# Kernel tuning notes

Hardware: AMD Instinct MI355X
Metric: run time of the kernel (lower is better)

The kernel has to match this reference:

```python
import jax, jax.numpy as jnp
import numpy as np

B, H, KV, HD, D, S = 8, 32, 8, 128, 4096, 4096
PAST = S - 2  # 4094, cache nearly full
ROPE_THETA = 10000.0


def rotate_half(x):
    h = x.shape[-1] // 2
    return jnp.concatenate([-x[..., h:], x[..., :h]], axis=-1)


def setup_inputs() -> dict:
    key = jax.random.key(0)
    ks = jax.random.split(key, 10)
    hidden_states = jax.random.normal(ks[0], (B, 1, D), jnp.float32)
    # HF additive causal mask for decode: 0 where position is valid, -inf-ish beyond
    pos = jnp.arange(S)
    attention_mask = jnp.broadcast_to(
        jnp.where(pos < PAST + 1, 0.0, -1e9).astype(jnp.float32)[None, None, None, :],
        (B, 1, 1, S),
    )
    # RoPE cos/sin for the single decoded position (position id = PAST)
    inv_freq = 1.0 / (ROPE_THETA ** (jnp.arange(0, HD, 2, dtype=jnp.float32) / HD))
    ang = PAST * inv_freq  # [HD/2]
    emb = jnp.concatenate([ang, ang], axis=-1)  # [HD]
    cos = jnp.broadcast_to(jnp.cos(emb)[None, None, :], (B, 1, HD)).astype(jnp.float32)
    sin = jnp.broadcast_to(jnp.sin(emb)[None, None, :], (B, 1, HD)).astype(jnp.float32)
    past_key = jax.random.normal(ks[1], (B, KV, PAST, HD), jnp.float32)
    past_value = jax.random.normal(ks[2], (B, KV, PAST, HD), jnp.float32)
    k_cache = jax.random.normal(ks[3], (B, KV, S, HD), jnp.float32)
    v_cache = jax.random.normal(ks[4], (B, KV, S, HD), jnp.float32)
    Wq = jax.random.normal(ks[5], (D, H * HD), jnp.float32) * 0.02
    Wk = jax.random.normal(ks[6], (D, KV * HD), jnp.float32) * 0.02
    Wv = jax.random.normal(ks[7], (D, KV * HD), jnp.float32) * 0.02
    Wo = jax.random.normal(ks[8], (H * HD, D), jnp.float32) * 0.02
    return dict(hidden_states=hidden_states, attention_mask=attention_mask, cos=cos,
                sin=sin, past_key=past_key, past_value=past_value,
                k_cache=k_cache, v_cache=v_cache, Wq=Wq, Wk=Wk, Wv=Wv, Wo=Wo)


def reference(hidden_states, attention_mask, cos, sin, past_key, past_value,
              k_cache, v_cache, Wq, Wk, Wv, Wo):
    b = hidden_states.shape[0]
    past_len = past_key.shape[2]  # static
    # q/k/v projections for the single decode token
    q = (hidden_states @ Wq).reshape(b, 1, H, HD).transpose(0, 2, 1, 3)   # [B,H,1,hd]
    k = (hidden_states @ Wk).reshape(b, 1, KV, HD).transpose(0, 2, 1, 3)  # [B,KV,1,hd]
    v = (hidden_states @ Wv).reshape(b, 1, KV, HD).transpose(0, 2, 1, 3)
    # rotary: cos/sin [B,1,hd] -> unsqueeze head dim -> [B,1,1,hd]
    c = cos[:, None, :, :]
    s = sin[:, None, :, :]
    q = q * c + rotate_half(q) * s
    k = k * c + rotate_half(k) * s
    # StaticCache: scatter past K/V into positions [0, past_len), new token at past_len
    kf = k_cache.at[:, :, :past_len, :].set(past_key)
    kf = kf.at[:, :, past_len:past_len + 1, :].set(k)
    vf = v_cache.at[:, :, :past_len, :].set(past_value)
    vf = vf.at[:, :, past_len:past_len + 1, :].set(v)
    # GQA: repeat kv heads
    n_rep = H // KV
    kr = jnp.repeat(kf, n_rep, axis=1)  # [B,H,S,hd]
    vr = jnp.repeat(vf, n_rep, axis=1)
    scores = jnp.einsum('bhqd,bhkd->bhqk', q, kr) / np.float32(np.sqrt(HD))
    scores = scores + attention_mask  # [B,1,1,S] broadcasts over heads
    probs = jax.nn.softmax(scores.astype(jnp.float32), axis=-1).astype(q.dtype)
    out = jnp.einsum('bhqk,bhkd->bhqd', probs, vr)  # [B,H,1,hd]
    out = out.transpose(0, 2, 1, 3).reshape(b, 1, H * HD)
    return out @ Wo  # [B,1,D]
```

## Files before the change

kernel.cpp:

```cpp
#include <hip/hip_runtime.h>

#define BB 8
#define HH 32
#define KVH 8
#define HD 128
#define DD 4096
#define PAST 4094
#define QCOLS 4096
#define KVCOLS 1024
#define NC_QKV 6144
#define DCH 64
#define NDCH 64
#define CHUNK 64
#define NCHUNK 64
#define QSCALE 0.08838834764831845f

__global__ __launch_bounds__(256)
void matvec_partial(const float* __restrict__ hin,
                    const float* __restrict__ W0,
                    const float* __restrict__ W1,
                    const float* __restrict__ W2,
                    int c_w1, int c_w2, int NC,
                    float* __restrict__ part)
{
    __shared__ float hl[DCH][BB];
    const int tid = threadIdx.x;
    const int d0 = blockIdx.y * DCH;
    const int cb = blockIdx.x * 512;

    for (int idx = tid; idx < DCH * BB; idx += 256) {
        int dd = idx & (DCH - 1);
        int b = idx >> 6;
        hl[dd][b] = hin[b * DD + d0 + dd];
    }
    __syncthreads();

    const int c = cb + tid * 2;
    const float* W;
    int ldw, cl;
    if (c < c_w1)      { W = W0; ldw = c_w1;        cl = c; }
    else if (c < c_w2) { W = W1; ldw = c_w2 - c_w1; cl = c - c_w1; }
    else               { W = W2; ldw = NC - c_w2;   cl = c - c_w2; }
    const float* wp = W + (size_t)d0 * ldw + cl;

    float2 acc[BB];
    #pragma unroll
    for (int b = 0; b < BB; ++b) { acc[b].x = 0.f; acc[b].y = 0.f; }

    #pragma unroll 8
    for (int dd = 0; dd < DCH; ++dd) {
        float2 w = *(const float2*)wp;
        wp += ldw;
        float hv[8];
        *(float4*)&hv[0] = *(const float4*)&hl[dd][0];
        *(float4*)&hv[4] = *(const float4*)&hl[dd][4];
        #pragma unroll
        for (int b = 0; b < BB; ++b) {
            acc[b].x = fmaf(hv[b], w.x, acc[b].x);
            acc[b].y = fmaf(hv[b], w.y, acc[b].y);
        }
    }

    float* po = part + (size_t)blockIdx.y * (BB * NC) + c;
    #pragma unroll
    for (int b = 0; b < BB; ++b) {
        *(float2*)(po + (size_t)b * NC) = acc[b];
    }
}

#define FIN_PER_B 3584
__global__ __launch_bounds__(256)
void qkv_finish(const float* __restrict__ part,
                const float* __restrict__ cosv,
                const float* __restrict__ sinv,
                float* __restrict__ qout,
                float* __restrict__ knew,
                float* __restrict__ vnew)
{
    const int idx = blockIdx.x * 256 + threadIdx.x;
    const int b = idx / FIN_PER_B;
    const int r = idx - b * FIN_PER_B;

    if (r < 2560) {
        const int hd = r & 63;
        const int head = r >> 6;
        const int c_lo = head * HD + hd;
        const float* p0 = part + (size_t)b * NC_QKV + c_lo;
        const float* p1 = p0 + 64;
        float s_lo = 0.f, s_hi = 0.f;
        #pragma unroll 8
        for (int i = 0; i < NDCH; ++i) {
            s_lo += p0[(size_t)i * (BB * NC_QKV)];
            s_hi += p1[(size_t)i * (BB * NC_QKV)];
        }
        const float cs_lo = cosv[b * HD + hd];
        const float sn_lo = sinv[b * HD + hd];
        const float cs_hi = cosv[b * HD + hd + 64];
        const float sn_hi = sinv[b * HD + hd + 64];
        const float v_lo = fmaf(s_lo, cs_lo, -s_hi * sn_lo);
        const float v_hi = fmaf(s_hi, cs_hi,  s_lo * sn_hi);
        if (c_lo < QCOLS) {
            qout[b * QCOLS + c_lo]      = v_lo * QSCALE;
            qout[b * QCOLS + c_lo + 64] = v_hi * QSCALE;
        } else {
            knew[b * KVCOLS + (c_lo - QCOLS)]      = v_lo;
            knew[b * KVCOLS + (c_lo - QCOLS) + 64] = v_hi;
        }
    } else {
        const int c = r - 2560 + QCOLS + KVCOLS;
        const float* p = part + (size_t)b * NC_QKV + c;
        float s = 0.f;
        #pragma unroll 8
        for (int i = 0; i < NDCH; ++i) s += p[(size_t)i * (BB * NC_QKV)];
        vnew[b * KVCOLS + (c - QCOLS - KVCOLS)] = s;
    }
}

__global__ __launch_bounds__(256)
void attn_partial(const float* __restrict__ past_key,
                  const float* __restrict__ past_value,
                  const float* __restrict__ q,
                  const float* __restrict__ knew,
                  const float* __restrict__ vnew,
                  float* __restrict__ pacc,
                  float* __restrict__ pl)
{
    const int pair = blockIdx.x;
    const int wid = threadIdx.x >> 6;
    const int chunk = blockIdx.y * 4 + wid;
    const int b = pair >> 3;
    const int kv = pair & 7;
    const int lane = threadIdx.x & 63;
    const int half = lane >> 5;
    const int lh = lane & 31;

    const float* qb = q + b * QCOLS + (kv * 4) * HD + 4 * lh;
    const float4 qv0 = *(const float4*)(qb);
    const float4 qv1 = *(const float4*)(qb + HD);
    const float4 qv2 = *(const float4*)(qb + 2 * HD);
    const float4 qv3 = *(const float4*)(qb + 3 * HD);

    const float* kb = past_key   + (size_t)pair * PAST * HD;
    const float* vb = past_value + (size_t)pair * PAST * HD;

    float4 acc0 = {0,0,0,0}, acc1 = {0,0,0,0}, acc2 = {0,0,0,0}, acc3 = {0,0,0,0};
    float l0 = 0.f, l1 = 0.f, l2 = 0.f, l3 = 0.f;

    const int jbase = chunk * CHUNK + half;

    if (chunk < NCHUNK - 1) {
        const float* kp = kb + (size_t)jbase * HD + 4 * lh;
        const float* vp = vb + (size_t)jbase * HD + 4 * lh;
        #pragma unroll 4
        for (int it = 0; it < 32; ++it) {
            const float4 kk = *(const float4*)kp;  kp += 2 * HD;
            float s0 = kk.x*qv0.x + kk.y*qv0.y + kk.z*qv0.z + kk.w*qv0.w;
            float s1 = kk.x*qv1.x + kk.y*qv1.y + kk.z*qv1.z + kk.w*qv1.w;
            float s2 = kk.x*qv2.x + kk.y*qv2.y + kk.z*qv2.z + kk.w*qv2.w;
            float s3 = kk.x*qv3.x + kk.y*qv3.y + kk.z*qv3.z + kk.w*qv3.w;
            #pragma unroll
            for (int m = 1; m <= 16; m <<= 1) {
                s0 += __shfl_xor(s0, m, 64);
                s1 += __shfl_xor(s1, m, 64);
                s2 += __shfl_xor(s2, m, 64);
                s3 += __shfl_xor(s3, m, 64);
            }
            const float4 vv = *(const float4*)vp;  vp += 2 * HD;
            const float p0 = __expf(s0);
            const float p1 = __expf(s1);
            const float p2 = __expf(s2);
            const float p3 = __expf(s3);
            l0 += p0; l1 += p1; l2 += p2; l3 += p3;
            acc0.x = fmaf(p0, vv.x, acc0.x); acc0.y = fmaf(p0, vv.y, acc0.y);
            acc0.z = fmaf(p0, vv.z, acc0.z); acc0.w = fmaf(p0, vv.w, acc0.w);
            acc1.x = fmaf(p1, vv.x, acc1.x); acc1.y = fmaf(p1, vv.y, acc1.y);
            acc1.z = fmaf(p1, vv.z, acc1.z); acc1.w = fmaf(p1, vv.w, acc1.w);
            acc2.x = fmaf(p2, vv.x, acc2.x); acc2.y = fmaf(p2, vv.y, acc2.y);
            acc2.z = fmaf(p2, vv.z, acc2.z); acc2.w = fmaf(p2, vv.w, acc2.w);
            acc3.x = fmaf(p3, vv.x, acc3.x); acc3.y = fmaf(p3, vv.y, acc3.y);
            acc3.z = fmaf(p3, vv.z, acc3.z); acc3.w = fmaf(p3, vv.w, acc3.w);
        }
    } else {
        const float* kn = knew + pair * HD;
        const float* vn = vnew + pair * HD;
        #pragma unroll 2
        for (int it = 0; it < 32; ++it) {
            const int j = jbase + it * 2;
            const bool valid = (j <= PAST);
            const float* kp;
            const float* vp;
            if (j < PAST) { kp = kb + (size_t)j * HD; vp = vb + (size_t)j * HD; }
            else          { kp = kn;                   vp = vn; }

            const float4 kk = *(const float4*)(kp + 4 * lh);
            float s0 = kk.x*qv0.x + kk.y*qv0.y + kk.z*qv0.z + kk.w*qv0.w;
            float s1 = kk.x*qv1.x + kk.y*qv1.y + kk.z*qv1.z + kk.w*qv1.w;
            float s2 = kk.x*qv2.x + kk.y*qv2.y + kk.z*qv2.z + kk.w*qv2.w;
            float s3 = kk.x*qv3.x + kk.y*qv3.y + kk.z*qv3.z + kk.w*qv3.w;
            #pragma unroll
            for (int m = 1; m <= 16; m <<= 1) {
                s0 += __shfl_xor(s0, m, 64);
                s1 += __shfl_xor(s1, m, 64);
                s2 += __shfl_xor(s2, m, 64);
                s3 += __shfl_xor(s3, m, 64);
            }
            const float4 vv = *(const float4*)(vp + 4 * lh);
            const float p0 = valid ? __expf(s0) : 0.f;
            const float p1 = valid ? __expf(s1) : 0.f;
            const float p2 = valid ? __expf(s2) : 0.f;
            const float p3 = valid ? __expf(s3) : 0.f;
            l0 += p0; l1 += p1; l2 += p2; l3 += p3;
            acc0.x = fmaf(p0, vv.x, acc0.x); acc0.y = fmaf(p0, vv.y, acc0.y);
            acc0.z = fmaf(p0, vv.z, acc0.z); acc0.w = fmaf(p0, vv.w, acc0.w);
            acc1.x = fmaf(p1, vv.x, acc1.x); acc1.y = fmaf(p1, vv.y, acc1.y);
            acc1.z = fmaf(p1, vv.z, acc1.z); acc1.w = fmaf(p1, vv.w, acc1.w);
            acc2.x = fmaf(p2, vv.x, acc2.x); acc2.y = fmaf(p2, vv.y, acc2.y);
            acc2.z = fmaf(p2, vv.z, acc2.z); acc2.w = fmaf(p2, vv.w, acc2.w);
            acc3.x = fmaf(p3, vv.x, acc3.x); acc3.y = fmaf(p3, vv.y, acc3.y);
            acc3.z = fmaf(p3, vv.z, acc3.z); acc3.w = fmaf(p3, vv.w, acc3.w);
        }
    }

    l0 += __shfl_xor(l0, 32, 64);
    l1 += __shfl_xor(l1, 32, 64);
    l2 += __shfl_xor(l2, 32, 64);
    l3 += __shfl_xor(l3, 32, 64);
    acc0.x += __shfl_xor(acc0.x, 32, 64); acc0.y += __shfl_xor(acc0.y, 32, 64);
    acc0.z += __shfl_xor(acc0.z, 32, 64); acc0.w += __shfl_xor(acc0.w, 32, 64);
    acc1.x += __shfl_xor(acc1.x, 32, 64); acc1.y += __shfl_xor(acc1.y, 32, 64);
    acc1.z += __shfl_xor(acc1.z, 32, 64); acc1.w += __shfl_xor(acc1.w, 32, 64);
    acc2.x += __shfl_xor(acc2.x, 32, 64); acc2.y += __shfl_xor(acc2.y, 32, 64);
    acc2.z += __shfl_xor(acc2.z, 32, 64); acc2.w += __shfl_xor(acc2.w, 32, 64);
    acc3.x += __shfl_xor(acc3.x, 32, 64); acc3.y += __shfl_xor(acc3.y, 32, 64);
    acc3.z += __shfl_xor(acc3.z, 32, 64); acc3.w += __shfl_xor(acc3.w, 32, 64);

    if (half == 0) {
        float* po = pacc + (((size_t)pair * NCHUNK + chunk) * 4) * HD + 4 * lh;
        *(float4*)(po)          = acc0;
        *(float4*)(po + HD)     = acc1;
        *(float4*)(po + 2*HD)   = acc2;
        *(float4*)(po + 3*HD)   = acc3;
        if (lh == 0) {
            float* plo = pl + ((size_t)pair * NCHUNK + chunk) * 4;
            plo[0] = l0; plo[1] = l1; plo[2] = l2; plo[3] = l3;
        }
    }
}

__global__ __launch_bounds__(256)
void attn_combine(const float* __restrict__ pacc,
                  const float* __restrict__ pl,
                  float* __restrict__ attn_out)
{
    const int idx = blockIdx.x * 256 + threadIdx.x;
    const int d = idx & 127;
    const int h = (idx >> 7) & 31;
    const int b = idx >> 12;
    const int kv = h >> 2;
    const int qi = h & 3;
    const int pair = b * 8 + kv;

    const float* pa  = pacc + (((size_t)pair * NCHUNK) * 4 + qi) * HD + d;
    const float* pls = pl + (size_t)pair * NCHUNK * 4 + qi;
    float acc = 0.f, lsum = 0.f;
    #pragma unroll 8
    for (int c = 0; c < NCHUNK; ++c) {
        acc  += pa[(size_t)c * 4 * HD];
        lsum += pls[c * 4];
    }
    attn_out[b * QCOLS + h * HD + d] = acc / lsum;
}

__global__ __launch_bounds__(256)
void wo_finish(const float* __restrict__ part, float* __restrict__ out)
{
    const int idx = blockIdx.x * 256 + threadIdx.x;
    float s = 0.f;
    #pragma unroll 8
    for (int i = 0; i < NDCH; ++i) s += part[(size_t)i * (BB * QCOLS) + idx];
    out[idx] = s;
}

extern "C" void kernel_launch(void* const* d_in, const int* in_sizes, int n_in,
                              void* d_out, int out_size, void* d_ws, size_t ws_size,
                              hipStream_t stream)
{
    (void)in_sizes; (void)n_in; (void)out_size; (void)ws_size;
    const float* hidden     = (const float*)d_in[0];
    const float* cosv       = (const float*)d_in[2];
    const float* sinv       = (const float*)d_in[3];
    const float* past_key   = (const float*)d_in[4];
    const float* past_value = (const float*)d_in[5];
    const float* Wq = (const float*)d_in[8];
    const float* Wk = (const float*)d_in[9];
    const float* Wv = (const float*)d_in[10];
    const float* Wo = (const float*)d_in[11];
    float* out = (float*)d_out;
    float* ws  = (float*)d_ws;

    float* qkv_part = ws;
    float* qrope    = qkv_part + (size_t)NDCH * BB * NC_QKV;
    float* knew     = qrope + BB * QCOLS;
    float* vnew     = knew + BB * KVCOLS;
    float* pacc     = vnew + BB * KVCOLS;
    float* pl       = pacc + (size_t)64 * NCHUNK * 4 * HD;
    float* attn_out = pl + (size_t)64 * NCHUNK * 4;
    float* wo_part  = qkv_part;

    matvec_partial<<<dim3(12, NDCH), 256, 0, stream>>>(
        hidden, Wq, Wk, Wv, 4096, 5120, NC_QKV, qkv_part);
    qkv_finish<<<(BB * FIN_PER_B) / 256, 256, 0, stream>>>(
        qkv_part, cosv, sinv, qrope, knew, vnew);
    attn_partial<<<dim3(64, NCHUNK / 4), 256, 0, stream>>>(
        past_key, past_value, qrope, knew, vnew, pacc, pl);
    attn_combine<<<(BB * HH * HD) / 256, 256, 0, stream>>>(pacc, pl, attn_out);
    matvec_partial<<<dim3(8, NDCH), 256, 0, stream>>>(
        attn_out, Wo, Wo, Wo, 4096, 5120, QCOLS, wo_part);
    wo_finish<<<(BB * QCOLS) / 256, 256, 0, stream>>>(wo_part, out);
}
```

Before: 111.7 us.

## Fuse attention combine into partial kernel via last-block counter, enlarge chunks

Removes the separate attn_combine launch: each attention block increments a per-pair atomic counter, and the last of the 8 blocks for that pair reduces the partial accumulators and writes the normalized output. The counter is reset inside qkv_finish. Chunk sizes for both the matvec reduction dimension and the attention sequence are doubled, which halves partial buffers and finish-kernel reads but also halves grid parallelism. wo_finish is vectorized to float4. The changes trade one kernel launch and partial-buffer traffic for fewer blocks in flight plus the fence and atomic overhead.

```diff
diff --git a/kernel.cpp b/kernel.cpp
--- a/kernel.cpp
+++ b/kernel.cpp
@@ -9,10 +9,10 @@
 #define QCOLS 4096
 #define KVCOLS 1024
 #define NC_QKV 6144
-#define DCH 64
-#define NDCH 64
-#define CHUNK 64
-#define NCHUNK 64
+#define DCH 128
+#define NDCH 32
+#define CHUNK 128
+#define NCHUNK 32
 #define QSCALE 0.08838834764831845f
 
 __global__ __launch_bounds__(256)
@@ -30,7 +30,7 @@
 
     for (int idx = tid; idx < DCH * BB; idx += 256) {
         int dd = idx & (DCH - 1);
-        int b = idx >> 6;
+        int b = idx >> 7;
         hl[dd][b] = hin[b * DD + d0 + dd];
     }
     __syncthreads();
@@ -47,7 +47,7 @@
     #pragma unroll
     for (int b = 0; b < BB; ++b) { acc[b].x = 0.f; acc[b].y = 0.f; }
 
-    #pragma unroll 8
+    #pragma unroll 16
     for (int dd = 0; dd < DCH; ++dd) {
         float2 w = *(const float2*)wp;
         wp += ldw;
@@ -75,8 +75,11 @@
                 const float* __restrict__ sinv,
                 float* __restrict__ qout,
                 float* __restrict__ knew,
-                float* __restrict__ vnew)
-{
+                float* __restrict__ vnew,
+                int* __restrict__ cnt)
+{
+    if (blockIdx.x == 0 && threadIdx.x < 64) cnt[threadIdx.x] = 0;
+
     const int idx = blockIdx.x * 256 + threadIdx.x;
     const int b = idx / FIN_PER_B;
     const int r = idx - b * FIN_PER_B;
@@ -123,7 +126,9 @@
                   const float* __restrict__ knew,
                   const float* __restrict__ vnew,
                   float* __restrict__ pacc,
-                  float* __restrict__ pl)
+                  float* __restrict__ pl,
+                  int* __restrict__ cnt,
+                  float* __restrict__ attn_out)
 {
     const int pair = blockIdx.x;
     const int wid = threadIdx.x >> 6;
@@ -152,7 +157,7 @@
         const float* kp = kb + (size_t)jbase * HD + 4 * lh;
         const float* vp = vb + (size_t)jbase * HD + 4 * lh;
         #pragma unroll 4
-        for (int it = 0; it < 32; ++it) {
+        for (int it = 0; it < 64; ++it) {
             const float4 kk = *(const float4*)kp;  kp += 2 * HD;
             float s0 = kk.x*qv0.x + kk.y*qv0.y + kk.z*qv0.z + kk.w*qv0.w;
             float s1 = kk.x*qv1.x + kk.y*qv1.y + kk.z*qv1.z + kk.w*qv1.w;
@@ -184,7 +189,7 @@
         const float* kn = knew + pair * HD;
         const float* vn = vnew + pair * HD;
         #pragma unroll 2
-        for (int it = 0; it < 32; ++it) {
+        for (int it = 0; it < 64; ++it) {
             const int j = jbase + it * 2;
             const bool valid = (j <= PAST);
             const float* kp;
@@ -245,40 +250,44 @@
             plo[0] = l0; plo[1] = l1; plo[2] = l2; plo[3] = l3;
         }
     }
-}
-
-__global__ __launch_bounds__(256)
-void attn_combine(const float* __restrict__ pacc,
-                  const float* __restrict__ pl,
-                  float* __restrict__ attn_out)
-{
-    const int idx = blockIdx.x * 256 + threadIdx.x;
-    const int d = idx & 127;
-    const int h = (idx >> 7) & 31;
-    const int b = idx >> 12;
-    const int kv = h >> 2;
-    const int qi = h & 3;
-    const int pair = b * 8 + kv;
-
-    const float* pa  = pacc + (((size_t)pair * NCHUNK) * 4 + qi) * HD + d;
-    const float* pls = pl + (size_t)pair * NCHUNK * 4 + qi;
-    float acc = 0.f, lsum = 0.f;
-    #pragma unroll 8
-    for (int c = 0; c < NCHUNK; ++c) {
-        acc  += pa[(size_t)c * 4 * HD];
-        lsum += pls[c * 4];
-    }
-    attn_out[b * QCOLS + h * HD + d] = acc / lsum;
+
+    __threadfence();
+    __syncthreads();
+    __shared__ int lastf;
+    if (threadIdx.x == 0) lastf = (atomicAdd(&cnt[pair], 1) == 7);
+    __syncthreads();
+    if (lastf) {
+        __threadfence();
+        const int qi = threadIdx.x >> 6;
+        const int dp = (threadIdx.x & 63) * 2;
+        const float* pa  = pacc + ((size_t)pair * NCHUNK * 4 + qi) * HD + dp;
+        const float* pls = pl + (size_t)pair * NCHUNK * 4 + qi;
+        float ax = 0.f, ay = 0.f, lsum = 0.f;
+        #pragma unroll 8
+        for (int ch = 0; ch < NCHUNK; ++ch) {
+            const float2 t = *(const float2*)(pa + (size_t)ch * 4 * HD);
+            ax += t.x; ay += t.y;
+            lsum += pls[ch * 4];
+        }
+        const float inv = 1.f / lsum;
+        float* ao = attn_out + b * QCOLS + (kv * 4 + qi) * HD + dp;
+        float2 r; r.x = ax * inv; r.y = ay * inv;
+        *(float2*)ao = r;
+    }
 }
 
 __global__ __launch_bounds__(256)
 void wo_finish(const float* __restrict__ part, float* __restrict__ out)
 {
     const int idx = blockIdx.x * 256 + threadIdx.x;
-    float s = 0.f;
+    const float* p = part + (size_t)idx * 4;
+    float4 s = {0.f, 0.f, 0.f, 0.f};
     #pragma unroll 8
-    for (int i = 0; i < NDCH; ++i) s += part[(size_t)i * (BB * QCOLS) + idx];
-    out[idx] = s;
+    for (int i = 0; i < NDCH; ++i) {
+        const float4 t = *(const float4*)(p + (size_t)i * (BB * QCOLS));
+        s.x += t.x; s.y += t.y; s.z += t.z; s.w += t.w;
+    }
+    *(float4*)(out + (size_t)idx * 4) = s;
 }
 
 extern "C" void kernel_launch(void* const* d_in, const int* in_sizes, int n_in,
@@ -305,16 +314,16 @@
     float* pacc     = vnew + BB * KVCOLS;
     float* pl       = pacc + (size_t)64 * NCHUNK * 4 * HD;
     float* attn_out = pl + (size_t)64 * NCHUNK * 4;
+    int*   cnt      = (int*)(attn_out + BB * QCOLS);
     float* wo_part  = qkv_part;
 
     matvec_partial<<<dim3(12, NDCH), 256, 0, stream>>>(
         hidden, Wq, Wk, Wv, 4096, 5120, NC_QKV, qkv_part);
     qkv_finish<<<(BB * FIN_PER_B) / 256, 256, 0, stream>>>(
-        qkv_part, cosv, sinv, qrope, knew, vnew);
+        qkv_part, cosv, sinv, qrope, knew, vnew, cnt);
     attn_partial<<<dim3(64, NCHUNK / 4), 256, 0, stream>>>(
-        past_key, past_value, qrope, knew, vnew, pacc, pl);
-    attn_combine<<<(BB * HH * HD) / 256, 256, 0, stream>>>(pacc, pl, attn_out);
+        past_key, past_value, qrope, knew, vnew, pacc, pl, cnt, attn_out);
     matvec_partial<<<dim3(8, NDCH), 256, 0, stream>>>(
         attn_out, Wo, Wo, Wo, 4096, 5120, QCOLS, wo_part);
-    wo_finish<<<(BB * QCOLS) / 256, 256, 0, stream>>>(wo_part, out);
-}
+    wo_finish<<<(BB * QCOLS / 4) / 256, 256, 0, stream>>>(wo_part, out);
+}
```

Result: slower. 215.4 us (+92.9%).

## Restructure decode attention to one query head per 16-lane group, larger chunks

Applied to the files above, without the earlier changes.

The attention partial kernel now gives each 16-lane group one query head, and each lane holds 8 elements of head_dim. Previously each wave split keys across two halves, with every lane carrying all four GQA heads. Each lane now processes one key row per iteration, which shortens the shuffle reduction to 4 steps and removes the cross-half reduction and the per-row bounds check. Chunks grow to 128 keys, halving the number of partial results that attn_combine must merge; the new token is handled as a separate tail step. wo_finish is vectorised to float4 with a quarter of the threads, and unroll factors are raised in qkv_finish.

```diff
diff --git a/kernel.cpp b/kernel.cpp
--- a/kernel.cpp
+++ b/kernel.cpp
@@ -11,8 +11,8 @@
 #define NC_QKV 6144
 #define DCH 64
 #define NDCH 64
-#define CHUNK 64
-#define NCHUNK 64
+#define CHUNK 128
+#define NCHUNK 32
 #define QSCALE 0.08838834764831845f
 
 __global__ __launch_bounds__(256)
@@ -88,7 +88,7 @@
         const float* p0 = part + (size_t)b * NC_QKV + c_lo;
         const float* p1 = p0 + 64;
         float s_lo = 0.f, s_hi = 0.f;
-        #pragma unroll 8
+        #pragma unroll 16
         for (int i = 0; i < NDCH; ++i) {
             s_lo += p0[(size_t)i * (BB * NC_QKV)];
             s_hi += p1[(size_t)i * (BB * NC_QKV)];
@@ -110,7 +110,7 @@
         const int c = r - 2560 + QCOLS + KVCOLS;
         const float* p = part + (size_t)b * NC_QKV + c;
         float s = 0.f;
-        #pragma unroll 8
+        #pragma unroll 16
         for (int i = 0; i < NDCH; ++i) s += p[(size_t)i * (BB * NC_QKV)];
         vnew[b * KVCOLS + (c - QCOLS - KVCOLS)] = s;
     }
@@ -131,119 +131,72 @@
     const int b = pair >> 3;
     const int kv = pair & 7;
     const int lane = threadIdx.x & 63;
-    const int half = lane >> 5;
-    const int lh = lane & 31;
-
-    const float* qb = q + b * QCOLS + (kv * 4) * HD + 4 * lh;
-    const float4 qv0 = *(const float4*)(qb);
-    const float4 qv1 = *(const float4*)(qb + HD);
-    const float4 qv2 = *(const float4*)(qb + 2 * HD);
-    const float4 qv3 = *(const float4*)(qb + 3 * HD);
+    const int g = lane >> 4;
+    const int i = lane & 15;
+
+    const float* qb = q + b * QCOLS + (kv * 4 + g) * HD + 8 * i;
+    const float4 qa = *(const float4*)(qb);
+    const float4 qc = *(const float4*)(qb + 4);
 
     const float* kb = past_key   + (size_t)pair * PAST * HD;
     const float* vb = past_value + (size_t)pair * PAST * HD;
 
-    float4 acc0 = {0,0,0,0}, acc1 = {0,0,0,0}, acc2 = {0,0,0,0}, acc3 = {0,0,0,0};
-    float l0 = 0.f, l1 = 0.f, l2 = 0.f, l3 = 0.f;
-
-    const int jbase = chunk * CHUNK + half;
-
-    if (chunk < NCHUNK - 1) {
-        const float* kp = kb + (size_t)jbase * HD + 4 * lh;
-        const float* vp = vb + (size_t)jbase * HD + 4 * lh;
-        #pragma unroll 4
-        for (int it = 0; it < 32; ++it) {
-            const float4 kk = *(const float4*)kp;  kp += 2 * HD;
-            float s0 = kk.x*qv0.x + kk.y*qv0.y + kk.z*qv0.z + kk.w*qv0.w;
-            float s1 = kk.x*qv1.x + kk.y*qv1.y + kk.z*qv1.z + kk.w*qv1.w;
-            float s2 = kk.x*qv2.x + kk.y*qv2.y + kk.z*qv2.z + kk.w*qv2.w;
-            float s3 = kk.x*qv3.x + kk.y*qv3.y + kk.z*qv3.z + kk.w*qv3.w;
-            #pragma unroll
-            for (int m = 1; m <= 16; m <<= 1) {
-                s0 += __shfl_xor(s0, m, 64);
-                s1 += __shfl_xor(s1, m, 64);
-                s2 += __shfl_xor(s2, m, 64);
-                s3 += __shfl_xor(s3, m, 64);
-            }
-            const float4 vv = *(const float4*)vp;  vp += 2 * HD;
-            const float p0 = __expf(s0);
-            const float p1 = __expf(s1);
-            const float p2 = __expf(s2);
-            const float p3 = __expf(s3);
-            l0 += p0; l1 += p1; l2 += p2; l3 += p3;
-            acc0.x = fmaf(p0, vv.x, acc0.x); acc0.y = fmaf(p0, vv.y, acc0.y);
-            acc0.z = fmaf(p0, vv.z, acc0.z); acc0.w = fmaf(p0, vv.w, acc0.w);
-            acc1.x = fmaf(p1, vv.x, acc1.x); acc1.y = fmaf(p1, vv.y, acc1.y);
-            acc1.z = fmaf(p1, vv.z, acc1.z); acc1.w = fmaf(p1, vv.w, acc1.w);
-            acc2.x = fmaf(p2, vv.x, acc2.x); acc2.y = fmaf(p2, vv.y, acc2.y);
-            acc2.z = fmaf(p2, vv.z, acc2.z); acc2.w = fmaf(p2, vv.w, acc2.w);
-            acc3.x = fmaf(p3, vv.x, acc3.x); acc3.y = fmaf(p3, vv.y, acc3.y);
-            acc3.z = fmaf(p3, vv.z, acc3.z); acc3.w = fmaf(p3, vv.w, acc3.w);
-        }
-    } else {
-        const float* kn = knew + pair * HD;
-        const float* vn = vnew + pair * HD;
-        #pragma unroll 2
-        for (int it = 0; it < 32; ++it) {
-            const int j = jbase + it * 2;
-            const bool valid = (j <= PAST);
-            const float* kp;
-            const float* vp;
-            if (j < PAST) { kp = kb + (size_t)j * HD; vp = vb + (size_t)j * HD; }
-            else          { kp = kn;                   vp = vn; }
-
-            const float4 kk = *(const float4*)(kp + 4 * lh);
-            float s0 = kk.x*qv0.x + kk.y*qv0.y + kk.z*qv0.z + kk.w*qv0.w;
-            float s1 = kk.x*qv1.x + kk.y*qv1.y + kk.z*qv1.z + kk.w*qv1.w;
-            float s2 = kk.x*qv2.x + kk.y*qv2.y + kk.z*qv2.z + kk.w*qv2.w;
-            float s3 = kk.x*qv3.x + kk.y*qv3.y + kk.z*qv3.z + kk.w*qv3.w;
-            #pragma unroll
-            for (int m = 1; m <= 16; m <<= 1) {
-                s0 += __shfl_xor(s0, m, 64);
-                s1 += __shfl_xor(s1, m, 64);
-                s2 += __shfl_xor(s2, m, 64);
-                s3 += __shfl_xor(s3, m, 64);
-            }
-            const float4 vv = *(const float4*)(vp + 4 * lh);
-            const float p0 = valid ? __expf(s0) : 0.f;
-            const float p1 = valid ? __expf(s1) : 0.f;
-            const float p2 = valid ? __expf(s2) : 0.f;
-            const float p3 = valid ? __expf(s3) : 0.f;
-            l0 += p0; l1 += p1; l2 += p2; l3 += p3;
-            acc0.x = fmaf(p0, vv.x, acc0.x); acc0.y = fmaf(p0, vv.y, acc0.y);
-            acc0.z = fmaf(p0, vv.z, acc0.z); acc0.w = fmaf(p0, vv.w, acc0.w);
-            acc1.x = fmaf(p1, vv.x, acc1.x); acc1.y = fmaf(p1, vv.y, acc1.y);
-            acc1.z = fmaf(p1, vv.z, acc1.z); acc1.w = fmaf(p1, vv.w, acc1.w);
-            acc2.x = fmaf(p2, vv.x, acc2.x); acc2.y = fmaf(p2, vv.y, acc2.y);
-            acc2.z = fmaf(p2, vv.z, acc2.z); acc2.w = fmaf(p2, vv.w, acc2.w);
-            acc3.x = fmaf(p3, vv.x, acc3.x); acc3.y = fmaf(p3, vv.y, acc3.y);
-            acc3.z = fmaf(p3, vv.z, acc3.z); acc3.w = fmaf(p3, vv.w, acc3.w);
-        }
-    }
-
-    l0 += __shfl_xor(l0, 32, 64);
-    l1 += __shfl_xor(l1, 32, 64);
-    l2 += __shfl_xor(l2, 32, 64);
-    l3 += __shfl_xor(l3, 32, 64);
-    acc0.x += __shfl_xor(acc0.x, 32, 64); acc0.y += __shfl_xor(acc0.y, 32, 64);
-    acc0.z += __shfl_xor(acc0.z, 32, 64); acc0.w += __shfl_xor(acc0.w, 32, 64);
-    acc1.x += __shfl_xor(acc1.x, 32, 64); acc1.y += __shfl_xor(acc1.y, 32, 64);
-    acc1.z += __shfl_xor(acc1.z, 32, 64); acc1.w += __shfl_xor(acc1.w, 32, 64);
-    acc2.x += __shfl_xor(acc2.x, 32, 64); acc2.y += __shfl_xor(acc2.y, 32, 64);
-    acc2.z += __shfl_xor(acc2.z, 32, 64); acc2.w += __shfl_xor(acc2.w, 32, 64);
-    acc3.x += __shfl_xor(acc3.x, 32, 64); acc3.y += __shfl_xor(acc3.y, 32, 64);
-    acc3.z += __shfl_xor(acc3.z, 32, 64); acc3.w += __shfl_xor(acc3.w, 32, 64);
-
-    if (half == 0) {
-        float* po = pacc + (((size_t)pair * NCHUNK + chunk) * 4) * HD + 4 * lh;
-        *(float4*)(po)          = acc0;
-        *(float4*)(po + HD)     = acc1;
-        *(float4*)(po + 2*HD)   = acc2;
-        *(float4*)(po + 3*HD)   = acc3;
-        if (lh == 0) {
-            float* plo = pl + ((size_t)pair * NCHUNK + chunk) * 4;
-            plo[0] = l0; plo[1] = l1; plo[2] = l2; plo[3] = l3;
-        }
+    float4 aa = {0,0,0,0}, ac = {0,0,0,0};
+    float l = 0.f;
+
+    const int jbase = chunk * CHUNK;
+    const float* kp = kb + (size_t)jbase * HD + 8 * i;
+    const float* vp = vb + (size_t)jbase * HD + 8 * i;
+
+    const int nit = (chunk < NCHUNK - 1) ? CHUNK : (CHUNK - 2);
+    #pragma unroll 4
+    for (int it = 0; it < nit; ++it) {
+        const float4 ka = *(const float4*)kp;
+        const float4 kc = *(const float4*)(kp + 4);
+        kp += HD;
+        float s = ka.x*qa.x + ka.y*qa.y + ka.z*qa.z + ka.w*qa.w
+                + kc.x*qc.x + kc.y*qc.y + kc.z*qc.z + kc.w*qc.w;
+        s += __shfl_xor(s, 1, 64);
+        s += __shfl_xor(s, 2, 64);
+        s += __shfl_xor(s, 4, 64);
+        s += __shfl_xor(s, 8, 64);
+        const float4 va = *(const float4*)vp;
+        const float4 vc = *(const float4*)(vp + 4);
+        vp += HD;
+        const float p = __expf(s);
+        l += p;
+        aa.x = fmaf(p, va.x, aa.x); aa.y = fmaf(p, va.y, aa.y);
+        aa.z = fmaf(p, va.z, aa.z); aa.w = fmaf(p, va.w, aa.w);
+        ac.x = fmaf(p, vc.x, ac.x); ac.y = fmaf(p, vc.y, ac.y);
+        ac.z = fmaf(p, vc.z, ac.z); ac.w = fmaf(p, vc.w, ac.w);
+    }
+
+    if (chunk == NCHUNK - 1) {
+        const float* kn = knew + pair * HD + 8 * i;
+        const float* vn = vnew + pair * HD + 8 * i;
+        const float4 ka = *(const float4*)kn;
+        const float4 kc = *(const float4*)(kn + 4);
+        float s = ka.x*qa.x + ka.y*qa.y + ka.z*qa.z + ka.w*qa.w
+                + kc.x*qc.x + kc.y*qc.y + kc.z*qc.z + kc.w*qc.w;
+        s += __shfl_xor(s, 1, 64);
+        s += __shfl_xor(s, 2, 64);
+        s += __shfl_xor(s, 4, 64);
+        s += __shfl_xor(s, 8, 64);
+        const float4 va = *(const float4*)vn;
+        const float4 vc = *(const float4*)(vn + 4);
+        const float p = __expf(s);
+        l += p;
+        aa.x = fmaf(p, va.x, aa.x); aa.y = fmaf(p, va.y, aa.y);
+        aa.z = fmaf(p, va.z, aa.z); aa.w = fmaf(p, va.w, aa.w);
+        ac.x = fmaf(p, vc.x, ac.x); ac.y = fmaf(p, vc.y, ac.y);
+        ac.z = fmaf(p, vc.z, ac.z); ac.w = fmaf(p, vc.w, ac.w);
+    }
+
+    float* po = pacc + (((size_t)pair * NCHUNK + chunk) * 4 + g) * HD + 8 * i;
+    *(float4*)(po)     = aa;
+    *(float4*)(po + 4) = ac;
+    if (i == 0) {
+        pl[((size_t)pair * NCHUNK + chunk) * 4 + g] = l;
     }
 }
 
@@ -260,7 +213,7 @@
     const int qi = h & 3;
     const int pair = b * 8 + kv;
 
-    const float* pa  = pacc + (((size_t)pair * NCHUNK) * 4 + qi) * HD + d;
+    const float* pa  = pacc + ((size_t)pair * NCHUNK * 4 + qi) * HD + d;
     const float* pls = pl + (size_t)pair * NCHUNK * 4 + qi;
     float acc = 0.f, lsum = 0.f;
     #pragma unroll 8
@@ -275,10 +228,14 @@
 void wo_finish(const float* __restrict__ part, float* __restrict__ out)
 {
     const int idx = blockIdx.x * 256 + threadIdx.x;
-    float s = 0.f;
-    #pragma unroll 8
-    for (int i = 0; i < NDCH; ++i) s += part[(size_t)i * (BB * QCOLS) + idx];
-    out[idx] = s;
+    const float* p = part + (size_t)idx * 4;
+    float4 s = {0.f, 0.f, 0.f, 0.f};
+    #pragma unroll 16
+    for (int i = 0; i < NDCH; ++i) {
+        const float4 t = *(const float4*)(p + (size_t)i * (BB * QCOLS));
+        s.x += t.x; s.y += t.y; s.z += t.z; s.w += t.w;
+    }
+    *(float4*)(out + (size_t)idx * 4) = s;
 }
 
 extern "C" void kernel_launch(void* const* d_in, const int* in_sizes, int n_in,
@@ -316,5 +273,5 @@
     attn_combine<<<(BB * HH * HD) / 256, 256, 0, stream>>>(pacc, pl, attn_out);
     matvec_partial<<<dim3(8, NDCH), 256, 0, stream>>>(
         attn_out, Wo, Wo, Wo, 4096, 5120, QCOLS, wo_part);
-    wo_finish<<<(BB * QCOLS) / 256, 256, 0, stream>>>(wo_part, out);
-}
+    wo_finish<<<(BB * QCOLS / 4) / 256, 256, 0, stream>>>(wo_part, out);
+}
```

After: 115.1 us. 3.0% more time.
